# Kernel optimization log

Measured on AMD Instinct MI355X. Metric: run time of the kernel, lower is better.

Reference implementation:

```python
import jax, jax.numpy as jnp
import numpy as np

N_EMBD = 1024
N_HEAD = 16
B, T, T_MEM = 4, 1024, 1024


def setup_inputs() -> dict:
    key = jax.random.key(0)
    ks = jax.random.split(key, 11)
    s = 1.0 / np.sqrt(N_EMBD)
    inp = {
        "q_in": jax.random.normal(ks[0], (B, T, N_EMBD), jnp.float32),
        "k_in": jax.random.normal(ks[1], (B, T_MEM, N_EMBD), jnp.float32),
        "v_in": jax.random.normal(ks[2], (B, T_MEM, N_EMBD), jnp.float32),
        "Wq": jax.random.normal(ks[3], (N_EMBD, N_EMBD), jnp.float32) * s,
        "bq": jnp.zeros((N_EMBD,), jnp.float32),
        "Wk": jax.random.normal(ks[4], (N_EMBD, N_EMBD), jnp.float32) * s,
        "bk": jnp.zeros((N_EMBD,), jnp.float32),
        "Wv": jax.random.normal(ks[5], (N_EMBD, N_EMBD), jnp.float32) * s,
        "bv": jnp.zeros((N_EMBD,), jnp.float32),
        "Wo": jax.random.normal(ks[6], (N_EMBD, N_EMBD), jnp.float32) * s,
        "bo": jnp.zeros((N_EMBD,), jnp.float32),
    }
    return inp


def reference(q_in, k_in, v_in, Wq, bq, Wk, bk, Wv, bv, Wo, bo):
    b, t, c = q_in.shape
    t_mem = k_in.shape[1]
    h = N_HEAD
    hs = c // h
    # torch Linear: x @ W.T + b
    q = (q_in @ Wq.T + bq).reshape(b, t, h, hs).transpose(0, 2, 1, 3)      # [b,h,t,hs]
    k = (k_in @ Wk.T + bk).reshape(b, t_mem, h, hs).transpose(0, 2, 1, 3)  # [b,h,tm,hs]
    v = (v_in @ Wv.T + bv).reshape(b, t_mem, h, hs).transpose(0, 2, 1, 3)
    att = jnp.einsum('bhtd,bhsd->bhts', q, k) * (1.0 / np.sqrt(hs))        # [b,h,t,tm]
    att = jax.nn.softmax(att, axis=-1)
    # dropout is identity (pdrop=0 / eval mode)
    y = jnp.einsum('bhts,bhsd->bhtd', att, v)                              # [b,h,t,hs]
    y = y.transpose(0, 2, 1, 3).reshape(b, t, c)
    y = y @ Wo.T + bo
    attention = att.mean(axis=1)                                           # [b,t,tm]
    return (y, attention)
```

## Files before the change

kernel.cpp:

```cpp
#include <hip/hip_runtime.h>

typedef unsigned short ushort_t;
typedef __attribute__((ext_vector_type(8))) __bf16 bf16x8;
typedef __attribute__((ext_vector_type(4))) float f32x4;

#define GLD(src, lds) __builtin_amdgcn_global_load_lds( \
    (const __attribute__((address_space(1))) void*)(src), \
    (__attribute__((address_space(3))) void*)(lds), 16, 0, 0)

#if __has_builtin(__builtin_amdgcn_exp2f)
#define EXP2(x) __builtin_amdgcn_exp2f(x)
#else
#define EXP2(x) __expf((x) * 0.69314718f)
#endif
#define QK_SCALE 0.18033688f

static __device__ __forceinline__ f32x4 mfma16(bf16x8 a, bf16x8 b, f32x4 c){
  return __builtin_amdgcn_mfma_f32_16x16x32_bf16(a, b, c, 0, 0, 0);
}
static __device__ __forceinline__ ushort_t f2bf(float f){
  unsigned u = __float_as_uint(f);
  return (ushort_t)((u + 0x7FFFu + ((u >> 16) & 1u)) >> 16);
}

template<int ROWS>
static __device__ __forceinline__ void stage64(const ushort_t* __restrict__ g, size_t rstride,
                                               ushort_t* lds, int tid){
#pragma unroll
  for (int r = 0; r < ROWS/32; ++r){
    int li = r*256 + tid;
    int row = li >> 3, ch = li & 7;
    GLD(g + (size_t)row*rstride + ((ch ^ (row & 7)) << 3),
        (char*)lds + (r*256 + (tid >> 6)*64)*16);
  }
}
static __device__ __forceinline__ bf16x8 frag64(const ushort_t* lds, int row, int ch){
  return *(const bf16x8*)((const char*)lds + row*128 + ((ch ^ (row & 7)) << 4));
}

static __device__ __forceinline__ void stage32(const ushort_t* __restrict__ g, size_t rstride,
                                               ushort_t* lds, int tid){
#pragma unroll
  for (int r = 0; r < 2; ++r){
    int li = r*256 + tid;
    int row = li >> 2, ch = li & 3;
    GLD(g + (size_t)row*rstride + ((ch ^ ((row >> 1) & 3)) << 3),
        (char*)lds + (r*256 + (tid >> 6)*64)*16);
  }
}
static __device__ __forceinline__ bf16x8 frag32(const ushort_t* lds, int row, int ch){
  return *(const bf16x8*)((const char*)lds + row*64 + ((ch ^ ((row >> 1) & 3)) << 4));
}

static __device__ __forceinline__ void stageA(const float* __restrict__ g, size_t rstride,
                                              float* lds, int tid){
#pragma unroll
  for (int r = 0; r < 4; ++r){
    int li = r*256 + tid;
    int row = li >> 3, ch = li & 7;
    GLD(g + (size_t)row*rstride + ((ch ^ (row & 7)) << 2),
        (char*)lds + (r*256 + (tid >> 6)*64)*16);
  }
}
static __device__ __forceinline__ bf16x8 fragA(const float* lds, int row, int fq){
  const char* base = (const char*)lds + row*128;
  f32x4 a = *(const f32x4*)(base + (((2*fq)     ^ (row & 7)) << 4));
  f32x4 b = *(const f32x4*)(base + (((2*fq + 1) ^ (row & 7)) << 4));
  bf16x8 o;
  o[0] = (__bf16)a[0]; o[1] = (__bf16)a[1]; o[2] = (__bf16)a[2]; o[3] = (__bf16)a[3];
  o[4] = (__bf16)b[0]; o[5] = (__bf16)b[1]; o[6] = (__bf16)b[2]; o[7] = (__bf16)b[3];
  return o;
}

__global__ __launch_bounds__(256) void cast_w(const float* __restrict__ wq,
    const float* __restrict__ wk, const float* __restrict__ wv,
    const float* __restrict__ wo, char* __restrict__ ws)
{
  const size_t MB = 1024*1024;
  int i = blockIdx.x*256 + threadIdx.x;
  int w = i >> 18, j = i & 262143;
  const float* src = w==0 ? wq : w==1 ? wk : w==2 ? wv : wo;
  ushort_t* dst = (ushort_t*)(ws + (24 + 2*(size_t)w)*MB);
  float4 x = ((const float4*)src)[j];
  ushort4 o;
  o.x = f2bf(x.x); o.y = f2bf(x.y); o.z = f2bf(x.z); o.w = f2bf(x.w);
  ((ushort4*)dst)[j] = o;
}

static __device__ __forceinline__ void gemm_f32_body(const float* __restrict__ A,
    const ushort_t* __restrict__ B, const float* __restrict__ bias,
    void* __restrict__ Cout, int bx, int mode, char* smem)
{
  constexpr int K = 1024;
  float*    As0 = (float*)smem;
  float*    As1 = (float*)(smem + 16384);
  ushort_t* Bs0 = (ushort_t*)(smem + 32768);
  ushort_t* Bs1 = (ushort_t*)(smem + 40960);
  const int tid = threadIdx.x, lane = tid & 63, wv = tid >> 6;
  const int fr = lane & 15, fq = lane >> 4;
  const int wr = wv >> 1, wc = wv & 1;
  const int brow0 = ((bx & 7) * 4 + ((bx >> 3) & 3)) * 128;
  const int bcol0 = (bx >> 5) * 128;

  const f32x4 zero = {0.f, 0.f, 0.f, 0.f};
  f32x4 acc[4][4];
#pragma unroll
  for (int m = 0; m < 4; ++m)
#pragma unroll
    for (int n = 0; n < 4; ++n) acc[m][n] = zero;

  stageA(A + (size_t)brow0*K, K, As0, tid);
  stage32(B + (size_t)bcol0*K, K, Bs0, tid);
  __syncthreads();

  for (int kt = 0; kt < K/32; ++kt){
    const int cur = kt & 1;
    float*    Ac = cur ? As1 : As0;
    ushort_t* Bc = cur ? Bs1 : Bs0;
    float*    An = cur ? As0 : As1;
    ushort_t* Bn = cur ? Bs0 : Bs1;
    if (kt < K/32 - 1){
      stageA(A + (size_t)brow0*K + (kt+1)*32, K, An, tid);
      stage32(B + (size_t)bcol0*K + (kt+1)*32, K, Bn, tid);
    }
    bf16x8 af[4], bfg[4];
#pragma unroll
    for (int m = 0; m < 4; ++m) af[m]  = fragA(Ac, wr*64 + m*16 + fr, fq);
#pragma unroll
    for (int n = 0; n < 4; ++n) bfg[n] = frag32(Bc, wc*64 + n*16 + fr, fq);
    __builtin_amdgcn_s_setprio(1);
#pragma unroll
    for (int m = 0; m < 4; ++m)
#pragma unroll
      for (int n = 0; n < 4; ++n)
        acc[m][n] = mfma16(af[m], bfg[n], acc[m][n]);
    __builtin_amdgcn_s_setprio(0);
    __syncthreads();
  }

#pragma unroll
  for (int n = 0; n < 4; ++n){
    const int colg = bcol0 + wc*64 + n*16 + fr;
    const float bv = bias[colg];
#pragma unroll
    for (int m = 0; m < 4; ++m){
      const int rowg0 = brow0 + wr*64 + m*16 + fq*4;
      if (mode == 1){
        int b = rowg0 >> 10, t = rowg0 & 1023, h = colg >> 6, d = colg & 63;
        ushort4 o;
        o.x = f2bf(acc[m][n][0] + bv); o.y = f2bf(acc[m][n][1] + bv);
        o.z = f2bf(acc[m][n][2] + bv); o.w = f2bf(acc[m][n][3] + bv);
        *(ushort4*)((ushort_t*)Cout + (((size_t)(b*16 + h))*64 + d)*1024 + t) = o;
      } else {
#pragma unroll
        for (int r = 0; r < 4; ++r){
          const int rowg = rowg0 + r;
          float val = acc[m][n][r] + bv;
          int b = rowg >> 10, t = rowg & 1023, h = colg >> 6, d = colg & 63;
          ((ushort_t*)Cout)[(((size_t)(b*16 + h))*1024 + t)*64 + d] = f2bf(val);
        }
      }
    }
  }
}

__global__ __launch_bounds__(256) void gemm_qkv(const float* q, const float* k,
    const float* v, const ushort_t* wqb, const ushort_t* wkb, const ushort_t* wvb,
    const float* bq, const float* bk, const float* bv,
    ushort_t* Qm, ushort_t* Km, ushort_t* Vtm)
{
  __shared__ char smem[49152];
  int id = blockIdx.x >> 8, bx = blockIdx.x & 255;
  const float* A = id==0 ? q : id==1 ? k : v;
  const ushort_t* B = id==0 ? wqb : id==1 ? wkb : wvb;
  const float* bias = id==0 ? bq : id==1 ? bk : bv;
  void* C = id==0 ? (void*)Qm : id==1 ? (void*)Km : (void*)Vtm;
  gemm_f32_body(A, B, bias, C, bx, id==2 ? 1 : 0, smem);
}

static __device__ __forceinline__ void gemm_body(const ushort_t* __restrict__ A,
    const ushort_t* __restrict__ B, const float* __restrict__ bias,
    void* __restrict__ Cout, int bx, char* smem)
{
  constexpr int K = 1024;
  const int tid = threadIdx.x, lane = tid & 63, wv = tid >> 6;
  const int fr = lane & 15, fq = lane >> 4;
  const int wr = wv >> 1, wc = wv & 1;
  const int brow0 = ((bx & 7) * 4 + ((bx >> 3) & 3)) * 128;
  const int bcol0 = (bx >> 5) * 128;

  const f32x4 zero = {0.f, 0.f, 0.f, 0.f};
  f32x4 acc[4][4];
#pragma unroll
  for (int m = 0; m < 4; ++m)
#pragma unroll
    for (int n = 0; n < 4; ++n) acc[m][n] = zero;

  const ushort_t* Abase = A + (size_t)brow0*K;
  const ushort_t* Bbase = B + (size_t)bcol0*K;

  stage32(Abase,      K, (ushort_t*)(smem),             tid);
  stage32(Bbase,      K, (ushort_t*)(smem + 24576),     tid);
  stage32(Abase + 32, K, (ushort_t*)(smem + 8192),      tid);
  stage32(Bbase + 32, K, (ushort_t*)(smem + 24576 + 8192), tid);
  asm volatile("s_waitcnt vmcnt(4)" ::: "memory");
  __builtin_amdgcn_s_barrier();

  int rd = 0, wrb = 2;
  for (int kt = 0; kt < 32; ++kt){
    if (kt < 30){
      stage32(Abase + (kt+2)*32, K, (ushort_t*)(smem + wrb*8192),         tid);
      stage32(Bbase + (kt+2)*32, K, (ushort_t*)(smem + 24576 + wrb*8192), tid);
    }
    const ushort_t* Ac = (const ushort_t*)(smem + rd*8192);
    const ushort_t* Bc = (const ushort_t*)(smem + 24576 + rd*8192);
    bf16x8 af[4], bfg[4];
#pragma unroll
    for (int m = 0; m < 4; ++m) af[m]  = frag32(Ac, wr*64 + m*16 + fr, fq);
#pragma unroll
    for (int n = 0; n < 4; ++n) bfg[n] = frag32(Bc, wc*64 + n*16 + fr, fq);
    __builtin_amdgcn_s_setprio(1);
#pragma unroll
    for (int m = 0; m < 4; ++m)
#pragma unroll
      for (int n = 0; n < 4; ++n)
        acc[m][n] = mfma16(af[m], bfg[n], acc[m][n]);
    __builtin_amdgcn_s_setprio(0);
    __builtin_amdgcn_sched_barrier(0);
    if (kt < 30) asm volatile("s_waitcnt vmcnt(4)" ::: "memory");
    else         asm volatile("s_waitcnt vmcnt(0)" ::: "memory");
    __builtin_amdgcn_s_barrier();
    rd  = (rd  == 2) ? 0 : rd  + 1;
    wrb = (wrb == 2) ? 0 : wrb + 1;
  }

#pragma unroll
  for (int n = 0; n < 4; ++n){
    const int colg = bcol0 + wc*64 + n*16 + fr;
    const float bv = bias[colg];
#pragma unroll
    for (int m = 0; m < 4; ++m){
      const int rowg0 = brow0 + wr*64 + m*16 + fq*4;
#pragma unroll
      for (int r = 0; r < 4; ++r){
        const int rowg = rowg0 + r;
        ((float*)Cout)[(size_t)rowg*1024 + colg] = acc[m][n][r] + bv;
      }
    }
  }
}

static __device__ __forceinline__ void attmean_body(const ushort_t* __restrict__ Q,
    const ushort_t* __restrict__ Kmat, const float* __restrict__ Lrow,
    float* __restrict__ attOut, int nb, char* smem)
{
  ushort_t* Qs0 = (ushort_t*)smem;
  ushort_t* Qs1 = (ushort_t*)(smem + 8192);
  ushort_t* Ks0 = (ushort_t*)(smem + 16384);
  ushort_t* Ks1 = (ushort_t*)(smem + 32768);
  const int tid = threadIdx.x, lane = tid & 63, wv = tid >> 6;
  const int fr = lane & 15, fq = lane >> 4;
  const int c_ = nb & 7, k_ = nb >> 3;
  const int b = c_ >> 1;
  const int rem = (c_ & 1)*64 + k_;
  const int t0 = (rem >> 3) * 64, s0 = (rem & 7) * 128;

  const f32x4 zero = {0.f, 0.f, 0.f, 0.f};
  f32x4 acc[2][4];
#pragma unroll
  for (int c = 0; c < 2; ++c)
#pragma unroll
    for (int n = 0; n < 4; ++n) acc[c][n] = zero;

  stage64<64>(Q + ((size_t)(b*16)*1024 + t0)*64, 64, Qs0, tid);
  stage64<128>(Kmat + ((size_t)(b*16)*1024 + s0)*64, 64, Ks0, tid);
  __syncthreads();

  for (int h = 0; h < 16; ++h){
    const int cur = h & 1;
    ushort_t* Qc = cur ? Qs1 : Qs0;
    ushort_t* Kc = cur ? Ks1 : Ks0;
    ushort_t* Qn = cur ? Qs0 : Qs1;
    ushort_t* Kn = cur ? Ks0 : Ks1;
    if (h < 15){
      stage64<64>(Q + ((size_t)(b*16 + h+1)*1024 + t0)*64, 64, Qn, tid);
      stage64<128>(Kmat + ((size_t)(b*16 + h+1)*1024 + s0)*64, 64, Kn, tid);
    }
    const int bh = b*16 + h;
    bf16x8 qf0 = frag64(Qc, wv*16 + fr, fq);
    bf16x8 qf1 = frag64(Qc, wv*16 + fr, 4 + fq);
    const float il = 1.f / Lrow[bh*1024 + t0 + wv*16 + fr];
#pragma unroll
    for (int c = 0; c < 2; ++c){
      f32x4 sfr[4];
      __builtin_amdgcn_s_setprio(1);
#pragma unroll
      for (int n = 0; n < 4; ++n){
        f32x4 s0v = mfma16(frag64(Kc, c*64 + n*16 + fr, fq), qf0, zero);
        sfr[n] = mfma16(frag64(Kc, c*64 + n*16 + fr, 4 + fq), qf1, s0v);
      }
      __builtin_amdgcn_s_setprio(0);
#pragma unroll
      for (int n = 0; n < 4; ++n)
#pragma unroll
        for (int r = 0; r < 4; ++r)
          acc[c][n][r] += EXP2(sfr[n][r] * QK_SCALE) * il;
    }
    __syncthreads();
  }

  const float s16 = 1.f/16.f;
#pragma unroll
  for (int c = 0; c < 2; ++c)
#pragma unroll
    for (int n = 0; n < 4; ++n){
      f32x4 v = acc[c][n];
      v[0] *= s16; v[1] *= s16; v[2] *= s16; v[3] *= s16;
      size_t idx = ((size_t)b << 20) + (size_t)(t0 + wv*16 + fr)*1024 + s0 + c*64 + n*16 + fq*4;
      *(f32x4*)(attOut + idx) = v;
    }
}

__global__ __launch_bounds__(256) void fused_tail(const ushort_t* __restrict__ Yws,
    const ushort_t* __restrict__ Wob, const float* __restrict__ bo, float* __restrict__ y_out,
    const ushort_t* __restrict__ Qm, const ushort_t* __restrict__ Km,
    const float* __restrict__ Lrow, float* __restrict__ att_out)
{
  __shared__ char smem[49152];
  const int bx = blockIdx.x;
  if (bx < 256) gemm_body(Yws, Wob, bo, y_out, bx, smem);
  else          attmean_body(Qm, Km, Lrow, att_out, bx - 256, smem);
}

__global__ __launch_bounds__(256, 2) void flash_kernel(const ushort_t* __restrict__ Q,
                                                       const ushort_t* __restrict__ Kmat,
                                                       const ushort_t* __restrict__ Vt,
                                                       ushort_t* __restrict__ Yws,
                                                       float* __restrict__ Lrow)
{
  __shared__ ushort_t Ks[2][64][64];
  __shared__ ushort_t Vts[2][64][64];
  __shared__ ushort_t Ps[4][32][64];
  const int tid = threadIdx.x, lane = tid & 63, wv = tid >> 6;
  const int fr = lane & 15, fq = lane >> 4;
  const int nb = blockIdx.x;
  const int bh = (nb & 7)*8 + (nb >> 6);
  const int t0 = ((nb >> 3) & 7) * 128;

  stage64<128>(Q + ((size_t)bh*1024 + t0)*64, 64, &Ps[0][0][0], tid);
  stage64<64>(Kmat + (size_t)bh*1024*64, 64, &Ks[0][0][0], tid);
  stage64<64>(Vt + (size_t)bh*64*1024, 1024, &Vts[0][0][0], tid);
  __syncthreads();
  bf16x8 aQ[2][2];
#pragma unroll
  for (int mt = 0; mt < 2; ++mt)
#pragma unroll
    for (int h = 0; h < 2; ++h)
      aQ[mt][h] = frag64(&Ps[0][0][0], wv*32 + mt*16 + fr, h*4 + fq);
  __syncthreads();

  bf16x8 ones;
#pragma unroll
  for (int i = 0; i < 8; ++i) ones[i] = (__bf16)1.0f;

  const f32x4 zero = {0.f, 0.f, 0.f, 0.f};
  f32x4 o_acc[2][4], l_acc[2];
#pragma unroll
  for (int mt = 0; mt < 2; ++mt){
    l_acc[mt] = zero;
#pragma unroll
    for (int n = 0; n < 4; ++n) o_acc[mt][n] = zero;
  }
  char* myP = (char*)&Ps[wv][0][0];

  for (int sc = 0; sc < 16; ++sc){
    const int cur = sc & 1;
    if (sc < 15){
      stage64<64>(Kmat + ((size_t)bh*1024 + (sc+1)*64)*64, 64, &Ks[cur^1][0][0], tid);
      stage64<64>(Vt + (size_t)bh*64*1024 + (sc+1)*64, 1024, &Vts[cur^1][0][0], tid);
    }
    bf16x8 kf[4][2];
#pragma unroll
    for (int n = 0; n < 4; ++n){
      kf[n][0] = frag64(&Ks[cur][0][0], n*16 + fr, fq);
      kf[n][1] = frag64(&Ks[cur][0][0], n*16 + fr, 4 + fq);
    }
    f32x4 sfr[2][4];
    __builtin_amdgcn_s_setprio(1);
#pragma unroll
    for (int mt = 0; mt < 2; ++mt)
#pragma unroll
      for (int n = 0; n < 4; ++n){
        f32x4 s0 = mfma16(kf[n][0], aQ[mt][0], zero);
        sfr[mt][n] = mfma16(kf[n][1], aQ[mt][1], s0);
      }
    __builtin_amdgcn_s_setprio(0);
#pragma unroll
    for (int mt = 0; mt < 2; ++mt){
#pragma unroll
      for (int n = 0; n < 4; ++n){
        float p0 = EXP2(sfr[mt][n][0] * QK_SCALE);
        float p1 = EXP2(sfr[mt][n][1] * QK_SCALE);
        float p2 = EXP2(sfr[mt][n][2] * QK_SCALE);
        float p3 = EXP2(sfr[mt][n][3] * QK_SCALE);
        uint2 w;
        w.x = (unsigned)f2bf(p0) | ((unsigned)f2bf(p1) << 16);
        w.y = (unsigned)f2bf(p2) | ((unsigned)f2bf(p3) << 16);
        *(uint2*)(myP + mt*2048 + fr*128 + (((n*4 + fq) ^ (fr & 14)) << 3)) = w;
      }
    }
    asm volatile("s_waitcnt lgkmcnt(0)" ::: "memory");
    __builtin_amdgcn_sched_barrier(0);
    __builtin_amdgcn_s_setprio(1);
#pragma unroll
    for (int ks = 0; ks < 2; ++ks){
      bf16x8 pa[2];
#pragma unroll
      for (int mt = 0; mt < 2; ++mt){
        uint4 u = *(const uint4*)(myP + mt*2048 + fr*128 + (((ks*8 + fq*2) ^ (fr & 14)) << 3));
        pa[mt] = __builtin_bit_cast(bf16x8, u);
      }
#pragma unroll
      for (int n = 0; n < 4; ++n){
        bf16x8 vf = frag64(&Vts[cur][0][0], n*16 + fr, ks*4 + fq);
#pragma unroll
        for (int mt = 0; mt < 2; ++mt)
          o_acc[mt][n] = mfma16(pa[mt], vf, o_acc[mt][n]);
      }
#pragma unroll
      for (int mt = 0; mt < 2; ++mt)
        l_acc[mt] = mfma16(pa[mt], ones, l_acc[mt]);
    }
    __builtin_amdgcn_s_setprio(0);
    __syncthreads();
  }

  const int b = bh >> 4, h = bh & 15;
#pragma unroll
  for (int mt = 0; mt < 2; ++mt){
    float inv[4];
#pragma unroll
    for (int r = 0; r < 4; ++r) inv[r] = 1.f / l_acc[mt][r];
#pragma unroll
    for (int n = 0; n < 4; ++n)
#pragma unroll
      for (int r = 0; r < 4; ++r){
        size_t row = (size_t)b*1024 + t0 + wv*32 + mt*16 + fq*4 + r;
        Yws[row*1024 + h*64 + n*16 + fr] = f2bf(o_acc[mt][n][r] * inv[r]);
      }
  }
  if (fr == 0){
#pragma unroll
    for (int mt = 0; mt < 2; ++mt)
#pragma unroll
      for (int r = 0; r < 4; ++r)
        Lrow[bh*1024 + t0 + wv*32 + mt*16 + fq*4 + r] = l_acc[mt][r];
  }
}

extern "C" void kernel_launch(void* const* d_in, const int* in_sizes, int n_in,
                              void* d_out, int out_size, void* d_ws, size_t ws_size,
                              hipStream_t stream)
{
  const float* q_in = (const float*)d_in[0];
  const float* k_in = (const float*)d_in[1];
  const float* v_in = (const float*)d_in[2];
  const float* Wq   = (const float*)d_in[3];
  const float* bq   = (const float*)d_in[4];
  const float* Wk   = (const float*)d_in[5];
  const float* bk   = (const float*)d_in[6];
  const float* Wv   = (const float*)d_in[7];
  const float* bv   = (const float*)d_in[8];
  const float* Wo   = (const float*)d_in[9];
  const float* bo   = (const float*)d_in[10];

  float* y_out   = (float*)d_out;
  float* att_out = y_out + (size_t)4*1024*1024;

  char* ws = (char*)d_ws;
  const size_t MB = 1024*1024;
  ushort_t* wqb  = (ushort_t*)(ws + 24*MB);
  ushort_t* wkb  = (ushort_t*)(ws + 26*MB);
  ushort_t* wvb  = (ushort_t*)(ws + 28*MB);
  ushort_t* wob  = (ushort_t*)(ws + 30*MB);
  ushort_t* Qm   = (ushort_t*)(ws + 32*MB);
  ushort_t* Km   = (ushort_t*)(ws + 40*MB);
  ushort_t* Vtm  = (ushort_t*)(ws + 48*MB);
  ushort_t* Yws  = (ushort_t*)(ws + 56*MB);
  float*    Lrow = (float*)(ws + 64*MB);

  cast_w<<<4096, 256, 0, stream>>>(Wq, Wk, Wv, Wo, ws);

  gemm_qkv<<<768, 256, 0, stream>>>(q_in, k_in, v_in, wqb, wkb, wvb,
                                    bq, bk, bv, Qm, Km, Vtm);

  flash_kernel<<<512, 256, 0, stream>>>(Qm, Km, Vtm, Yws, Lrow);

  fused_tail<<<768, 256, 0, stream>>>(Yws, wob, bo, y_out, Qm, Km, Lrow, att_out);
}
```

Before: 122.6 us.

## Stage fp32 A tiles through registers and store bf16 to LDS in QKV GEMM

The QKV projection GEMM used to copy fp32 activation tiles straight into LDS with global_load_lds and converted them to bf16 at every fragment read. It now loads the fp32 tile into registers, converts it to bf16 once, and writes it to a swizzled bf16 LDS buffer after the MFMA block, so the same frag32 read path serves both operands. LDS use drops from 48KB to 32KB, which can raise occupancy and halves the LDS traffic for A. The cost is extra VGPRs for the prefetch, and the global loads are now exposed through registers instead of being asynchronous direct-to-LDS copies.

```diff
diff --git a/kernel.cpp b/kernel.cpp
--- a/kernel.cpp
+++ b/kernel.cpp
@@ -52,24 +52,30 @@
   return *(const bf16x8*)((const char*)lds + row*64 + ((ch ^ ((row >> 1) & 3)) << 4));
 }
 
-static __device__ __forceinline__ void stageA(const float* __restrict__ g, size_t rstride,
-                                              float* lds, int tid){
-#pragma unroll
-  for (int r = 0; r < 4; ++r){
+static __device__ __forceinline__ void loadA_f32(const float* __restrict__ g,
+                                                 float4 (&d)[2][2], int tid){
+#pragma unroll
+  for (int r = 0; r < 2; ++r){
     int li = r*256 + tid;
-    int row = li >> 3, ch = li & 7;
-    GLD(g + (size_t)row*rstride + ((ch ^ (row & 7)) << 2),
-        (char*)lds + (r*256 + (tid >> 6)*64)*16);
-  }
-}
-static __device__ __forceinline__ bf16x8 fragA(const float* lds, int row, int fq){
-  const char* base = (const char*)lds + row*128;
-  f32x4 a = *(const f32x4*)(base + (((2*fq)     ^ (row & 7)) << 4));
-  f32x4 b = *(const f32x4*)(base + (((2*fq + 1) ^ (row & 7)) << 4));
-  bf16x8 o;
-  o[0] = (__bf16)a[0]; o[1] = (__bf16)a[1]; o[2] = (__bf16)a[2]; o[3] = (__bf16)a[3];
-  o[4] = (__bf16)b[0]; o[5] = (__bf16)b[1]; o[6] = (__bf16)b[2]; o[7] = (__bf16)b[3];
-  return o;
+    int row = li >> 2;
+    int lc = (li & 3) ^ ((row >> 1) & 3);
+    const float* s = g + (size_t)row*1024 + lc*8;
+    d[r][0] = ((const float4*)s)[0];
+    d[r][1] = ((const float4*)s)[1];
+  }
+}
+static __device__ __forceinline__ void commitA(const float4 (&d)[2][2],
+                                               ushort_t* lds, int tid){
+#pragma unroll
+  for (int r = 0; r < 2; ++r){
+    int li = r*256 + tid;
+    bf16x8 o;
+    o[0] = (__bf16)d[r][0].x; o[1] = (__bf16)d[r][0].y;
+    o[2] = (__bf16)d[r][0].z; o[3] = (__bf16)d[r][0].w;
+    o[4] = (__bf16)d[r][1].x; o[5] = (__bf16)d[r][1].y;
+    o[6] = (__bf16)d[r][1].z; o[7] = (__bf16)d[r][1].w;
+    *(bf16x8*)((char*)lds + li*16) = o;
+  }
 }
 
 __global__ __launch_bounds__(256) void cast_w(const float* __restrict__ wq,
@@ -92,10 +98,10 @@
     void* __restrict__ Cout, int bx, int mode, char* smem)
 {
   constexpr int K = 1024;
-  float*    As0 = (float*)smem;
-  float*    As1 = (float*)(smem + 16384);
-  ushort_t* Bs0 = (ushort_t*)(smem + 32768);
-  ushort_t* Bs1 = (ushort_t*)(smem + 40960);
+  ushort_t* As0 = (ushort_t*)smem;
+  ushort_t* As1 = (ushort_t*)(smem + 8192);
+  ushort_t* Bs0 = (ushort_t*)(smem + 16384);
+  ushort_t* Bs1 = (ushort_t*)(smem + 24576);
   const int tid = threadIdx.x, lane = tid & 63, wv = tid >> 6;
   const int fr = lane & 15, fq = lane >> 4;
   const int wr = wv >> 1, wc = wv & 1;
@@ -109,23 +115,25 @@
 #pragma unroll
     for (int n = 0; n < 4; ++n) acc[m][n] = zero;
 
-  stageA(A + (size_t)brow0*K, K, As0, tid);
+  float4 pfA[2][2];
+  loadA_f32(A + (size_t)brow0*K, pfA, tid);
+  commitA(pfA, As0, tid);
   stage32(B + (size_t)bcol0*K, K, Bs0, tid);
   __syncthreads();
 
   for (int kt = 0; kt < K/32; ++kt){
     const int cur = kt & 1;
-    float*    Ac = cur ? As1 : As0;
+    ushort_t* Ac = cur ? As1 : As0;
     ushort_t* Bc = cur ? Bs1 : Bs0;
-    float*    An = cur ? As0 : As1;
+    ushort_t* An = cur ? As0 : As1;
     ushort_t* Bn = cur ? Bs0 : Bs1;
     if (kt < K/32 - 1){
-      stageA(A + (size_t)brow0*K + (kt+1)*32, K, An, tid);
+      loadA_f32(A + (size_t)brow0*K + (kt+1)*32, pfA, tid);
       stage32(B + (size_t)bcol0*K + (kt+1)*32, K, Bn, tid);
     }
     bf16x8 af[4], bfg[4];
 #pragma unroll
-    for (int m = 0; m < 4; ++m) af[m]  = fragA(Ac, wr*64 + m*16 + fr, fq);
+    for (int m = 0; m < 4; ++m) af[m]  = frag32(Ac, wr*64 + m*16 + fr, fq);
 #pragma unroll
     for (int n = 0; n < 4; ++n) bfg[n] = frag32(Bc, wc*64 + n*16 + fr, fq);
     __builtin_amdgcn_s_setprio(1);
@@ -135,6 +143,8 @@
       for (int n = 0; n < 4; ++n)
         acc[m][n] = mfma16(af[m], bfg[n], acc[m][n]);
     __builtin_amdgcn_s_setprio(0);
+    if (kt < K/32 - 1)
+      commitA(pfA, An, tid);
     __syncthreads();
   }
 
@@ -169,7 +179,7 @@
     const float* bq, const float* bk, const float* bv,
     ushort_t* Qm, ushort_t* Km, ushort_t* Vtm)
 {
-  __shared__ char smem[49152];
+  __shared__ char smem[32768];
   int id = blockIdx.x >> 8, bx = blockIdx.x & 255;
   const float* A = id==0 ? q : id==1 ? k : v;
   const ushort_t* B = id==0 ? wqb : id==1 ? wkb : wvb;
```

Measured after the change: 119.6 us, median of 2. 2.4% less time.
